# Performance work log

Hardware: AMD Instinct MI355X
Metric: run time of the kernel (lower is better)

Reference implementation:

```python
import jax, jax.numpy as jnp
import numpy as np

E = 640000   # number of edges/messages
D = 128      # feature dim
N = 100000   # number of segments (nodes)


def setup_inputs() -> dict:
    key = jax.random.key(0)
    k1, k2 = jax.random.split(key)
    x = jax.random.normal(k1, (E, D), dtype=jnp.float32)
    index = jnp.sort(jax.random.randint(k2, (E,), 0, N, dtype=jnp.int64))
    return {"x": x, "index": index, "dim_size": N}


def reference(x, index, dim_size):
    # scatter_mean over dim=-2: sum rows of x into segments, divide by counts
    sums = jax.ops.segment_sum(x, index, num_segments=dim_size)            # [N, D]
    counts = jax.ops.segment_sum(jnp.ones((x.shape[0],), dtype=x.dtype),
                                 index, num_segments=dim_size)             # [N]
    counts = jnp.maximum(counts, 1.0)  # clamp(1) as in torch_scatter mean
    return sums / counts[:, None]
```

## Files before the change

kernel.cpp:

```cpp
#include <hip/hip_runtime.h>


#define FEAT_D   128
#define FEAT_D4  32

__global__ __launch_bounds__(256) void scatter_mean_fused(
        const float4* __restrict__ x4,
        const int*    __restrict__ index,
        float4*       __restrict__ out4,
        int E, int N) {
    int l    = threadIdx.x & 63;
    int wave = threadIdx.x >> 6;
    int n    = blockIdx.x * 4 + wave;
    if (n >= N) return;

    int sub  = l >> 5;
    int lane = l & 31;

    int target = n + sub;
    int lo = 0, hi = E;
    while (lo < hi) {
        int mid = (lo + hi) >> 1;
        if (index[mid] < target) lo = mid + 1; else hi = mid;
    }
    int start = __shfl(lo, 0, 64);
    int end   = __shfl(lo, 32, 64);

    float4 acc = make_float4(0.f, 0.f, 0.f, 0.f);
    for (int e = start + sub; e < end; e += 2) {
        float4 v = x4[(size_t)e * FEAT_D4 + lane];
        acc.x += v.x; acc.y += v.y; acc.z += v.z; acc.w += v.w;
    }

    acc.x += __shfl_down(acc.x, 32, 64);
    acc.y += __shfl_down(acc.y, 32, 64);
    acc.z += __shfl_down(acc.z, 32, 64);
    acc.w += __shfl_down(acc.w, 32, 64);

    if (sub == 0) {
        int c = end - start;
        float inv = 1.0f / (float)(c > 0 ? c : 1);
        acc.x *= inv; acc.y *= inv; acc.z *= inv; acc.w *= inv;
        out4[(size_t)n * FEAT_D4 + lane] = acc;
    }
}

extern "C" void kernel_launch(void* const* d_in, const int* in_sizes, int n_in,
                              void* d_out, int out_size, void* d_ws, size_t ws_size,
                              hipStream_t stream) {
    const float* x     = (const float*)d_in[0];
    const int*   index = (const int*)d_in[1];

    const int E = in_sizes[1];
    const int N = out_size / FEAT_D;

    int threads = 256;
    int blocks  = (N + 3) / 4;
    scatter_mean_fused<<<blocks, threads, 0, stream>>>(
        (const float4*)x, index, (float4*)d_out, E, N);
}
```

Before: 519.0 us.

## Process 64 segments per block with shared boundary search and 4-way edge split

Each block now handles 64 consecutive segments, computing the 65 segment boundaries once by binary search into shared memory instead of two searches per wave. Each wave loops over 16 segments, splitting a segment's edges across four 16-lane groups that each load two float4 per row, then reduces with xor shuffles. The aim is to cut redundant binary-search traffic and increase memory-level parallelism per row. In exchange there are fewer blocks, a block-wide barrier, and idle lanes in waves whose segments have few edges.

```diff
diff --git a/kernel.cpp b/kernel.cpp
--- a/kernel.cpp
+++ b/kernel.cpp
@@ -1,47 +1,77 @@
 #include <hip/hip_runtime.h>
 
 
-#define FEAT_D   128
-#define FEAT_D4  32
+#define SEGS 64
+#define D4   32
 
-__global__ __launch_bounds__(256) void scatter_mean_fused(
+__global__ __launch_bounds__(256) void scatter_mean_blk(
         const float4* __restrict__ x4,
         const int*    __restrict__ index,
         float4*       __restrict__ out4,
         int E, int N) {
-    int l    = threadIdx.x & 63;
-    int wave = threadIdx.x >> 6;
-    int n    = blockIdx.x * 4 + wave;
-    if (n >= N) return;
+    __shared__ int sOff[SEGS + 1];
+    const int base = blockIdx.x * SEGS;
+    const int t    = threadIdx.x;
 
-    int sub  = l >> 5;
-    int lane = l & 31;
+    for (int tt = t; tt <= SEGS; tt += 256) {
+        int target = base + tt;
+        int lo = 0, hi = E;
+        while (lo < hi) {
+            int mid = (lo + hi) >> 1;
+            if (index[mid] < target) lo = mid + 1; else hi = mid;
+        }
+        sOff[tt] = lo;
+    }
+    __syncthreads();
 
-    int target = n + sub;
-    int lo = 0, hi = E;
-    while (lo < hi) {
-        int mid = (lo + hi) >> 1;
-        if (index[mid] < target) lo = mid + 1; else hi = mid;
-    }
-    int start = __shfl(lo, 0, 64);
-    int end   = __shfl(lo, 32, 64);
+    const int wave = t >> 6;
+    const int l    = t & 63;
+    const int sub  = l >> 4;
+    const int lane = l & 15;
 
-    float4 acc = make_float4(0.f, 0.f, 0.f, 0.f);
-    for (int e = start + sub; e < end; e += 2) {
-        float4 v = x4[(size_t)e * FEAT_D4 + lane];
-        acc.x += v.x; acc.y += v.y; acc.z += v.z; acc.w += v.w;
-    }
+    for (int s = wave; s < SEGS; s += 4) {
+        const int n = base + s;
+        if (n >= N) break;
+        const int start = sOff[s];
+        const int end   = sOff[s + 1];
 
-    acc.x += __shfl_down(acc.x, 32, 64);
-    acc.y += __shfl_down(acc.y, 32, 64);
-    acc.z += __shfl_down(acc.z, 32, 64);
-    acc.w += __shfl_down(acc.w, 32, 64);
+        float4 a0 = make_float4(0.f, 0.f, 0.f, 0.f);
+        float4 a1 = make_float4(0.f, 0.f, 0.f, 0.f);
+        for (int e = start + sub; e < end; e += 4) {
+            const float4* p = x4 + (size_t)e * D4 + lane * 2;
+            float4 v0 = p[0];
+            float4 v1 = p[1];
+            a0.x += v0.x; a0.y += v0.y; a0.z += v0.z; a0.w += v0.w;
+            a1.x += v1.x; a1.y += v1.y; a1.z += v1.z; a1.w += v1.w;
+        }
 
-    if (sub == 0) {
-        int c = end - start;
-        float inv = 1.0f / (float)(c > 0 ? c : 1);
-        acc.x *= inv; acc.y *= inv; acc.z *= inv; acc.w *= inv;
-        out4[(size_t)n * FEAT_D4 + lane] = acc;
+        a0.x += __shfl_xor(a0.x, 16, 64);
+        a0.y += __shfl_xor(a0.y, 16, 64);
+        a0.z += __shfl_xor(a0.z, 16, 64);
+        a0.w += __shfl_xor(a0.w, 16, 64);
+        a1.x += __shfl_xor(a1.x, 16, 64);
+        a1.y += __shfl_xor(a1.y, 16, 64);
+        a1.z += __shfl_xor(a1.z, 16, 64);
+        a1.w += __shfl_xor(a1.w, 16, 64);
+
+        a0.x += __shfl_xor(a0.x, 32, 64);
+        a0.y += __shfl_xor(a0.y, 32, 64);
+        a0.z += __shfl_xor(a0.z, 32, 64);
+        a0.w += __shfl_xor(a0.w, 32, 64);
+        a1.x += __shfl_xor(a1.x, 32, 64);
+        a1.y += __shfl_xor(a1.y, 32, 64);
+        a1.z += __shfl_xor(a1.z, 32, 64);
+        a1.w += __shfl_xor(a1.w, 32, 64);
+
+        if (sub == 0) {
+            int c = end - start;
+            float inv = 1.0f / (float)(c > 0 ? c : 1);
+            a0.x *= inv; a0.y *= inv; a0.z *= inv; a0.w *= inv;
+            a1.x *= inv; a1.y *= inv; a1.z *= inv; a1.w *= inv;
+            float4* o = out4 + (size_t)n * D4 + lane * 2;
+            o[0] = a0;
+            o[1] = a1;
+        }
     }
 }
 
@@ -52,10 +82,9 @@
     const int*   index = (const int*)d_in[1];
 
     const int E = in_sizes[1];
-    const int N = out_size / FEAT_D;
+    const int N = out_size / 128;
 
-    int threads = 256;
-    int blocks  = (N + 3) / 4;
-    scatter_mean_fused<<<blocks, threads, 0, stream>>>(
+    int blocks = (N + SEGS - 1) / SEGS;
+    scatter_mean_blk<<<blocks, 256, 0, stream>>>(
         (const float4*)x, index, (float4*)d_out, E, N);
 }
```

Measured after the change: 461.7 us. 11.1% less time.

## Partition work by fixed edge chunks per wave instead of one segment per wave

Applied to the files above, without the earlier changes.

Each wave now owns a contiguous chunk of about 80 edges, aligned to segment boundaries by binary search. It streams the rows with a full 64-lane float2 read per edge and writes the mean whenever the segment id changes, zero-filling any empty segments in its range. This removes the per-segment binary searches and gives balanced work with fewer waves and full-width row loads. In exchange, each wave walks its edges serially, which lowers memory-level parallelism per wave, and a segment that spans many chunks is handled entirely by one wave.

```diff
diff --git a/kernel.cpp b/kernel.cpp
--- a/kernel.cpp
+++ b/kernel.cpp
@@ -1,48 +1,57 @@
 #include <hip/hip_runtime.h>
 
 
-#define FEAT_D   128
-#define FEAT_D4  32
+#define EPW 80
+#define D2  64
 
-__global__ __launch_bounds__(256) void scatter_mean_fused(
-        const float4* __restrict__ x4,
+__global__ __launch_bounds__(256) void scatter_mean_stream(
+        const float2* __restrict__ x2,
         const int*    __restrict__ index,
-        float4*       __restrict__ out4,
-        int E, int N) {
-    int l    = threadIdx.x & 63;
-    int wave = threadIdx.x >> 6;
-    int n    = blockIdx.x * 4 + wave;
-    if (n >= N) return;
+        float2*       __restrict__ out2,
+        int E, int N, int W) {
+    const int gwave = (int)((blockIdx.x * blockDim.x + threadIdx.x) >> 6);
+    if (gwave >= W) return;
+    const int l   = threadIdx.x & 63;
+    const int sub = l >> 5;
 
-    int sub  = l >> 5;
-    int lane = l & 31;
-
-    int target = n + sub;
+    int pe = (gwave + sub) * EPW;
+    int starget = (pe < E) ? index[pe] : N;
     int lo = 0, hi = E;
     while (lo < hi) {
         int mid = (lo + hi) >> 1;
-        if (index[mid] < target) lo = mid + 1; else hi = mid;
+        if (index[mid] < starget) lo = mid + 1; else hi = mid;
     }
-    int start = __shfl(lo, 0, 64);
-    int end   = __shfl(lo, 32, 64);
+    int e     = __shfl(lo, 0, 64);
+    int e_end = __shfl(lo, 32, 64);
+    int s_lo  = __shfl(starget, 0, 64);
+    int s_hi  = __shfl(starget, 32, 64);
 
-    float4 acc = make_float4(0.f, 0.f, 0.f, 0.f);
-    for (int e = start + sub; e < end; e += 2) {
-        float4 v = x4[(size_t)e * FEAT_D4 + lane];
-        acc.x += v.x; acc.y += v.y; acc.z += v.z; acc.w += v.w;
+    const float2 z = make_float2(0.f, 0.f);
+
+    if (gwave == 0) {
+        for (int g = 0; g < s_lo; ++g) out2[(size_t)g * D2 + l] = z;
     }
+    if (e >= e_end) return;
 
-    acc.x += __shfl_down(acc.x, 32, 64);
-    acc.y += __shfl_down(acc.y, 32, 64);
-    acc.z += __shfl_down(acc.z, 32, 64);
-    acc.w += __shfl_down(acc.w, 32, 64);
-
-    if (sub == 0) {
-        int c = end - start;
-        float inv = 1.0f / (float)(c > 0 ? c : 1);
-        acc.x *= inv; acc.y *= inv; acc.z *= inv; acc.w *= inv;
-        out4[(size_t)n * FEAT_D4 + lane] = acc;
+    int   cur = s_lo;
+    int   cnt = 0;
+    float2 acc = z;
+    for (; e < e_end; ++e) {
+        int seg = index[e];
+        if (seg != cur) {
+            float inv = 1.0f / (float)cnt;
+            out2[(size_t)cur * D2 + l] = make_float2(acc.x * inv, acc.y * inv);
+            for (int g = cur + 1; g < seg; ++g)
+                out2[(size_t)g * D2 + l] = z;
+            cur = seg; acc = z; cnt = 0;
+        }
+        float2 v = x2[(size_t)e * D2 + l];
+        acc.x += v.x; acc.y += v.y; ++cnt;
     }
+    float inv = 1.0f / (float)cnt;
+    out2[(size_t)cur * D2 + l] = make_float2(acc.x * inv, acc.y * inv);
+    for (int g = cur + 1; g < s_hi; ++g)
+        out2[(size_t)g * D2 + l] = z;
 }
 
 extern "C" void kernel_launch(void* const* d_in, const int* in_sizes, int n_in,
@@ -52,10 +61,11 @@
     const int*   index = (const int*)d_in[1];
 
     const int E = in_sizes[1];
-    const int N = out_size / FEAT_D;
+    const int N = out_size / 128;
 
-    int threads = 256;
-    int blocks  = (N + 3) / 4;
-    scatter_mean_fused<<<blocks, threads, 0, stream>>>(
-        (const float4*)x, index, (float4*)d_out, E, N);
+    const int W = (E + EPW - 1) / EPW;
+    const int threads = 256;
+    const int blocks  = (W * 64 + threads - 1) / threads;
+    scatter_mean_stream<<<blocks, threads, 0, stream>>>(
+        (const float2*)x, index, (float2*)d_out, E, N, W);
 }
```

Result: faster. 474.7 us (-8.5%).
